# Kernel optimization log

Measured on AMD Instinct MI355X. Metric: run time of the kernel, lower is better.

Reference implementation:

```python
import jax, jax.numpy as jnp
import numpy as np

N = 50000      # nodes
E = 800000     # edges (before self-loops)
HEADS = 4
IN = 128
HID = 96
DH = HID // HEADS  # 24 per-head channels
G = 64         # graphs in batch
OUT = 3


def setup_inputs() -> dict:
    key = jax.random.key(0)
    ks = jax.random.split(key, 16)
    def w(k, shape, fan):
        return (jax.random.normal(k, shape, jnp.float32) * (fan ** -0.5)).astype(jnp.float32)
    x = jax.random.normal(ks[0], (N, IN), jnp.float32)
    edge_index = jax.random.randint(ks[1], (2, E), 0, N, dtype=jnp.int32)
    batch = jnp.sort(jax.random.randint(ks[2], (N,), 0, G, dtype=jnp.int32))
    return {
        'x': x, 'edge_index': edge_index, 'batch': batch, 'num_graphs': G,
        'W1': w(ks[3], (IN, HID), IN),
        'att_src1': w(ks[4], (HEADS, DH), DH),
        'att_dst1': w(ks[5], (HEADS, DH), DH),
        'b1': jnp.zeros((HID,), jnp.float32),
        'W2': w(ks[6], (HID, HID), HID),
        'att_src2': w(ks[7], (HEADS, DH), DH),
        'att_dst2': w(ks[8], (HEADS, DH), DH),
        'b2': jnp.zeros((HID,), jnp.float32),
        'g_w1': w(ks[9], (HID, HID // 2), HID),
        'g_b1': jnp.zeros((HID // 2,), jnp.float32),
        'g_w2': w(ks[10], (HID // 2, 1), HID // 2),
        'g_b2': jnp.zeros((1,), jnp.float32),
        'f_w1': w(ks[11], (HID, HID), HID),
        'f_b1': jnp.zeros((HID,), jnp.float32),
        'f_w2': w(ks[12], (HID, OUT), HID),
        'f_b2': jnp.zeros((OUT,), jnp.float32),
    }


def _gat_layer(x, src, dst, W, a_src, a_dst, b, n):
    # x: [n, F]; src/dst: [E'] (self-loops included). PyG GATConv math.
    h = (x @ W).reshape(n, HEADS, DH)                 # [n, H, d]
    alpha_s = jnp.sum(h * a_src[None], axis=-1)       # [n, H]
    alpha_d = jnp.sum(h * a_dst[None], axis=-1)       # [n, H]
    e = jax.nn.leaky_relu(alpha_s[src] + alpha_d[dst], 0.2)  # [E', H]
    # segment softmax over incoming edges of each dst node
    m = jax.ops.segment_max(e, dst, num_segments=n)   # [n, H]
    ex = jnp.exp(e - m[dst])
    denom = jax.ops.segment_sum(ex, dst, num_segments=n)
    alpha = ex / (denom[dst] + 1e-16)                 # [E', H]
    msg = h[src] * alpha[:, :, None]                  # [E', H, d]
    out = jax.ops.segment_sum(msg, dst, num_segments=n)
    return out.reshape(n, HEADS * DH) + b


def reference(x, edge_index, batch, num_graphs, W1, att_src1, att_dst1, b1,
              W2, att_src2, att_dst2, b2, g_w1, g_b1, g_w2, g_b2,
              f_w1, f_b1, f_w2, f_b2):
    n = x.shape[0]
    loops = jnp.arange(n, dtype=edge_index.dtype)
    src = jnp.concatenate([edge_index[0], loops])     # add self-loops (PyG default)
    dst = jnp.concatenate([edge_index[1], loops])
    h = jax.nn.elu(_gat_layer(x, src, dst, W1, att_src1, att_dst1, b1, n))
    h = jax.nn.elu(_gat_layer(h, src, dst, W2, att_src2, att_dst2, b2, n))
    # GlobalAttention pool: gate_nn -> softmax over batch segments -> weighted sum
    gate = (jax.nn.relu(h @ g_w1 + g_b1) @ g_w2 + g_b2)[:, 0]   # [n]
    gm = jax.ops.segment_max(gate, batch, num_segments=num_graphs)
    gm = jnp.where(jnp.isfinite(gm), gm, 0.0)
    ge = jnp.exp(gate - gm[batch])
    gden = jax.ops.segment_sum(ge, batch, num_segments=num_graphs)
    wgt = ge / (gden[batch] + 1e-16)                  # [n]
    pooled = jax.ops.segment_sum(h * wgt[:, None], batch, num_segments=num_graphs)  # [G, HID]
    return jax.nn.relu(pooled @ f_w1 + f_b1) @ f_w2 + f_b2   # [G, 3]
```

## Files before the change

kernel.cpp:

```cpp
#include <hip/hip_runtime.h>
#include <cmath>


__global__ void init_deg_kernel(int* __restrict__ deg, int n) {
    int i = blockIdx.x * blockDim.x + threadIdx.x;
    if (i < n) deg[i] = 1;
}

__global__ void hist_kernel(const int* __restrict__ dst, int* __restrict__ deg, int E) {
    int e = blockIdx.x * blockDim.x + threadIdx.x;
    if (e < E) atomicAdd(&deg[dst[e]], 1);
}

__global__ void scan_bsum_kernel(const int* __restrict__ deg, int* __restrict__ bsum, int n) {
    __shared__ int s[256];
    int t = threadIdx.x;
    int base = blockIdx.x * 1024;
    int sum = 0;
#pragma unroll
    for (int j = 0; j < 4; j++) {
        int i = base + j * 256 + t;
        if (i < n) sum += deg[i];
    }
    s[t] = sum;
    __syncthreads();
    for (int off = 128; off; off >>= 1) {
        if (t < off) s[t] += s[t + off];
        __syncthreads();
    }
    if (t == 0) bsum[blockIdx.x] = s[0];
}

__global__ void scan_bsum_scan_kernel(int* __restrict__ bsum, int nb,
                                      int* __restrict__ rowptr, int n) {
    __shared__ int s[256];
    int t = threadIdx.x;
    int v = (t < nb) ? bsum[t] : 0;
    s[t] = v;
    __syncthreads();
    for (int off = 1; off < 256; off <<= 1) {
        int x = (t >= off) ? s[t - off] : 0;
        __syncthreads();
        s[t] += x;
        __syncthreads();
    }
    if (t < nb) bsum[t] = s[t] - v;
    if (t == 255) rowptr[n] = s[255];
}

__global__ void scan_local_kernel(const int* __restrict__ deg, const int* __restrict__ bsum,
                                  int* __restrict__ rowptr, int* __restrict__ pos, int n) {
    __shared__ int s[256];
    int t = threadIdx.x;
    int base = blockIdx.x * 1024;
    int d[4];
    int sum = 0;
#pragma unroll
    for (int j = 0; j < 4; j++) {
        int i = base + t * 4 + j;
        d[j] = (i < n) ? deg[i] : 0;
        sum += d[j];
    }
    s[t] = sum;
    __syncthreads();
    for (int off = 1; off < 256; off <<= 1) {
        int x = (t >= off) ? s[t - off] : 0;
        __syncthreads();
        s[t] += x;
        __syncthreads();
    }
    int run = bsum[blockIdx.x] + s[t] - sum;
#pragma unroll
    for (int j = 0; j < 4; j++) {
        int i = base + t * 4 + j;
        if (i < n) { rowptr[i] = run; pos[i] = run; }
        run += d[j];
    }
}

__global__ void fill_kernel(const int* __restrict__ src, const int* __restrict__ dst,
                            int* __restrict__ pos, int* __restrict__ col, int E, int N) {
    int i = blockIdx.x * blockDim.x + threadIdx.x;
    if (i < E) {
        int p = atomicAdd(&pos[dst[i]], 1);
        col[p] = src[i];
    } else if (i < E + N) {
        int n = i - E;
        int p = atomicAdd(&pos[n], 1);
        col[p] = n;
    }
}

template<int K, int NCOL, int TN, int MODE>
__global__ __launch_bounds__(256)
void tiled_gemm_kernel(const float* __restrict__ X, const float* __restrict__ W,
                       const float* __restrict__ v1, const float* __restrict__ v2,
                       const float* __restrict__ v3,
                       float* __restrict__ H, float* __restrict__ AS, float* __restrict__ AD,
                       int n_nodes) {
    const int t = threadIdx.x;
    const int tx = t & 15, ty = t >> 4;
    const int c0 = tx * TN;
    const int m0 = ty * 4;
    const int node0 = blockIdx.x * 64;

    __shared__ float As[16][68];
    __shared__ float Bs[16][NCOL];

    float acc[4][TN];
#pragma unroll
    for (int i = 0; i < 4; i++)
#pragma unroll
        for (int j = 0; j < TN; j++) acc[i][j] = 0.f;

    const int am = t >> 2, akq = t & 3;

    for (int kb = 0; kb < K; kb += 16) {
        float4 av = make_float4(0.f, 0.f, 0.f, 0.f);
        int anode = node0 + am;
        if (anode < n_nodes)
            av = *reinterpret_cast<const float4*>(X + (size_t)anode * K + kb + akq * 4);
        As[akq * 4 + 0][am] = av.x;
        As[akq * 4 + 1][am] = av.y;
        As[akq * 4 + 2][am] = av.z;
        As[akq * 4 + 3][am] = av.w;
        {
            const float4* wsrc = reinterpret_cast<const float4*>(W + (size_t)kb * NCOL);
            float4* bdst = reinterpret_cast<float4*>(&Bs[0][0]);
            for (int i = t; i < 16 * NCOL / 4; i += 256) bdst[i] = wsrc[i];
        }
        __syncthreads();
#pragma unroll
        for (int k = 0; k < 16; k++) {
            float4 a4 = *reinterpret_cast<const float4*>(&As[k][m0]);
            float a[4] = {a4.x, a4.y, a4.z, a4.w};
            float b[TN];
            if constexpr ((TN & 1) == 0) {
#pragma unroll
                for (int j = 0; j < TN / 2; j++) {
                    float2 b2 = *reinterpret_cast<const float2*>(&Bs[k][c0 + 2 * j]);
                    b[2 * j] = b2.x; b[2 * j + 1] = b2.y;
                }
            } else {
#pragma unroll
                for (int j = 0; j < TN; j++) b[j] = Bs[k][c0 + j];
            }
#pragma unroll
            for (int i = 0; i < 4; i++)
#pragma unroll
                for (int j = 0; j < TN; j++)
                    acc[i][j] = fmaf(a[i], b[j], acc[i][j]);
        }
        __syncthreads();
    }

    if constexpr (MODE == 0) {
        __shared__ float s_as[64][16];
        __shared__ float s_ad[64][16];
#pragma unroll
        for (int i = 0; i < 4; i++) {
            int node = node0 + m0 + i;
            float asp = 0.f, adp = 0.f;
#pragma unroll
            for (int j = 0; j < TN; j++) {
                asp = fmaf(acc[i][j], v1[c0 + j], asp);
                adp = fmaf(acc[i][j], v2[c0 + j], adp);
            }
            s_as[m0 + i][tx] = asp;
            s_ad[m0 + i][tx] = adp;
            if (node < n_nodes) {
#pragma unroll
                for (int j = 0; j < TN / 2; j++) {
                    float2 o;
                    o.x = acc[i][2 * j]; o.y = acc[i][2 * j + 1];
                    *reinterpret_cast<float2*>(H + (size_t)node * NCOL + c0 + 2 * j) = o;
                }
            }
        }
        __syncthreads();
        int m = t >> 2, head = t & 3;
        int node = node0 + m;
        if (node < n_nodes) {
            float s1 = s_as[m][head * 4 + 0] + s_as[m][head * 4 + 1]
                     + s_as[m][head * 4 + 2] + s_as[m][head * 4 + 3];
            float s2 = s_ad[m][head * 4 + 0] + s_ad[m][head * 4 + 1]
                     + s_ad[m][head * 4 + 2] + s_ad[m][head * 4 + 3];
            AS[(size_t)node * 4 + head] = s1;
            AD[(size_t)node * 4 + head] = s2;
        }
    } else {
        __shared__ float s_g[64][16];
#pragma unroll
        for (int i = 0; i < 4; i++) {
            float p = 0.f;
#pragma unroll
            for (int j = 0; j < TN; j++) {
                float a = acc[i][j] + v1[c0 + j];
                a = fmaxf(a, 0.f);
                p = fmaf(a, v2[c0 + j], p);
            }
            s_g[m0 + i][tx] = p;
        }
        __syncthreads();
        if (t < 64) {
            int node = node0 + t;
            if (node < n_nodes) {
                float s = 0.f;
#pragma unroll
                for (int j = 0; j < 16; j++) s += s_g[t][j];
                H[node] = s + v3[0];
            }
        }
    }
}

__global__ __launch_bounds__(256)
void gat_agg_wave_kernel(const float* __restrict__ H, const float* __restrict__ AS,
                         const float* __restrict__ AD, const int* __restrict__ rowptr,
                         const int* __restrict__ col, const float* __restrict__ bias,
                         float* __restrict__ OUT, int n_nodes) {
    int wid = threadIdx.x >> 6;
    int lane = threadIdx.x & 63;
    int n = blockIdx.x * 4 + wid;
    if (n >= n_nodes) return;
    int beg = rowptr[n];
    int deg = rowptr[n + 1] - beg;

    int h = lane & 3;
    int slot = lane >> 2;
    float ad_n = AD[(size_t)n * 4 + h];

    float mymax = -INFINITY;
    for (int i = slot; i < deg; i += 16) {
        int s = col[beg + i];
        float v = AS[(size_t)s * 4 + h] + ad_n;
        v = v > 0.f ? v : 0.2f * v;
        mymax = fmaxf(mymax, v);
    }
#pragma unroll
    for (int m = 4; m <= 32; m <<= 1)
        mymax = fmaxf(mymax, __shfl_xor(mymax, m, 64));
    float m_h = mymax;

    int c = lane;
    bool cown = c < 48;
    int head_c = cown ? (c / 12) : 0;
    const float2* __restrict__ Hc = reinterpret_cast<const float2*>(H) + c;

    float denom_part = 0.f;
    float2 acc0 = make_float2(0.f, 0.f), acc1 = make_float2(0.f, 0.f);
    float2 acc2 = make_float2(0.f, 0.f), acc3 = make_float2(0.f, 0.f);

    for (int base = 0; base < deg; base += 16) {
        int ce = base + slot;
        int s_e = 0;
        float ex = 0.f;
        if (ce < deg) {
            s_e = col[beg + ce];
            float v = AS[(size_t)s_e * 4 + h] + ad_n;
            v = v > 0.f ? v : 0.2f * v;
            ex = __expf(v - m_h);
        }
        denom_part += ex;
        int cnt = min(16, deg - base);

        int sbv[16];
        float wv[16];
#pragma unroll
        for (int i = 0; i < 16; i++) {
            sbv[i] = __shfl(s_e, i * 4, 64);
            wv[i]  = __shfl(ex,  i * 4 + head_c, 64);
        }

#pragma unroll
        for (int g = 0; g < 16; g += 4) {
            if (g < cnt && cown) {
                float2 v0 = Hc[(size_t)sbv[g + 0] * 48];
                float2 v1 = Hc[(size_t)sbv[g + 1] * 48];
                float2 v2 = Hc[(size_t)sbv[g + 2] * 48];
                float2 v3 = Hc[(size_t)sbv[g + 3] * 48];
                acc0.x = fmaf(v0.x, wv[g + 0], acc0.x);
                acc0.y = fmaf(v0.y, wv[g + 0], acc0.y);
                acc1.x = fmaf(v1.x, wv[g + 1], acc1.x);
                acc1.y = fmaf(v1.y, wv[g + 1], acc1.y);
                acc2.x = fmaf(v2.x, wv[g + 2], acc2.x);
                acc2.y = fmaf(v2.y, wv[g + 2], acc2.y);
                acc3.x = fmaf(v3.x, wv[g + 3], acc3.x);
                acc3.y = fmaf(v3.y, wv[g + 3], acc3.y);
            }
        }
    }

#pragma unroll
    for (int m = 4; m <= 32; m <<= 1)
        denom_part += __shfl_xor(denom_part, m, 64);
    float den = __shfl(denom_part, head_c, 64);

    if (cown) {
        float2 acc;
        acc.x = (acc0.x + acc1.x) + (acc2.x + acc3.x);
        acc.y = (acc0.y + acc1.y) + (acc2.y + acc3.y);
        float2 b2 = reinterpret_cast<const float2*>(bias)[c];
        float inv = 1.f / (den + 1e-16f);
        float ox = acc.x * inv + b2.x;
        float oy = acc.y * inv + b2.y;
        ox = ox > 0.f ? ox : (__expf(ox) - 1.f);
        oy = oy > 0.f ? oy : (__expf(oy) - 1.f);
        reinterpret_cast<float2*>(OUT)[(size_t)n * 48 + c] = make_float2(ox, oy);
    }
}

__device__ __forceinline__ int lower_bound_dev(const int* __restrict__ arr, int n, int key) {
    int lo = 0, hi = n;
    while (lo < hi) {
        int mid = (lo + hi) >> 1;
        if (arr[mid] < key) lo = mid + 1; else hi = mid;
    }
    return lo;
}

__global__ void gate_stats_kernel(const float* __restrict__ gate, const int* __restrict__ batch,
                                  int n_nodes, float* __restrict__ gm_out,
                                  float* __restrict__ inv_gden_out, float* __restrict__ pooled) {
    int g = blockIdx.x, t = threadIdx.x;
    if (t < 96) pooled[(size_t)g * 96 + t] = 0.f;
    __shared__ int sb, se;
    __shared__ float sred[256];
    if (t == 0) {
        sb = lower_bound_dev(batch, n_nodes, g);
        se = lower_bound_dev(batch, n_nodes, g + 1);
    }
    __syncthreads();
    int beg = sb, end = se;

    float mx = -INFINITY;
    for (int i = beg + t; i < end; i += 256) mx = fmaxf(mx, gate[i]);
    sred[t] = mx;
    __syncthreads();
    for (int off = 128; off; off >>= 1) {
        if (t < off) sred[t] = fmaxf(sred[t], sred[t + off]);
        __syncthreads();
    }
    float gm = sred[0];
    if (!isfinite(gm)) gm = 0.f;
    __syncthreads();

    float sm = 0.f;
    for (int i = beg + t; i < end; i += 256) sm += __expf(gate[i] - gm);
    sred[t] = sm;
    __syncthreads();
    for (int off = 128; off; off >>= 1) {
        if (t < off) sred[t] += sred[t + off];
        __syncthreads();
    }
    if (t == 0) {
        gm_out[g] = gm;
        inv_gden_out[g] = 1.f / (sred[0] + 1e-16f);
    }
}

__global__ __launch_bounds__(384)
void pool_accum_kernel(const float* __restrict__ H2, const float* __restrict__ gate,
                       const int* __restrict__ batch, const float* __restrict__ gm,
                       const float* __restrict__ inv_gden, int n_nodes,
                       float* __restrict__ pooled) {
    const int NPB = 256;
    int t = threadIdx.x;
    int group = t / 96;
    int c = t - group * 96;
    if (group >= 4) return;
    int nbeg = blockIdx.x * NPB;
    int nend = min(nbeg + NPB, n_nodes);

    float acc = 0.f;
    int curg = -1;
    for (int i = nbeg + group; i < nend; i += 4) {
        int g = batch[i];
        if (g != curg) {
            if (curg >= 0) atomicAdd(&pooled[(size_t)curg * 96 + c], acc);
            acc = 0.f;
            curg = g;
        }
        float w = __expf(gate[i] - gm[curg]) * inv_gden[curg];
        acc = fmaf(w, H2[(size_t)i * 96 + c], acc);
    }
    if (curg >= 0) atomicAdd(&pooled[(size_t)curg * 96 + c], acc);
}

__global__ void final_kernel(const float* __restrict__ pooled, const float* __restrict__ f_w1,
                             const float* __restrict__ f_b1, const float* __restrict__ f_w2,
                             const float* __restrict__ f_b2, float* __restrict__ out) {
    int g = blockIdx.x, t = threadIdx.x;
    __shared__ float sp[96], sh[96];
    sp[t] = pooled[(size_t)g * 96 + t];
    __syncthreads();
    float a = f_b1[t];
    for (int k = 0; k < 96; k++) a = fmaf(sp[k], f_w1[k * 96 + t], a);
    sh[t] = fmaxf(a, 0.f);
    __syncthreads();
    if (t < 3) {
        float o = f_b2[t];
        for (int k = 0; k < 96; k++) o = fmaf(sh[k], f_w2[k * 3 + t], o);
        out[g * 3 + t] = o;
    }
}

extern "C" void kernel_launch(void* const* d_in, const int* in_sizes, int n_in,
                              void* d_out, int out_size, void* d_ws, size_t ws_size,
                              hipStream_t stream) {
    const float* x    = (const float*)d_in[0];
    const int*   ei   = (const int*)d_in[1];
    const int*   batch= (const int*)d_in[2];
    const float* W1   = (const float*)d_in[4];
    const float* as1  = (const float*)d_in[5];
    const float* ad1  = (const float*)d_in[6];
    const float* b1   = (const float*)d_in[7];
    const float* W2   = (const float*)d_in[8];
    const float* as2  = (const float*)d_in[9];
    const float* ad2  = (const float*)d_in[10];
    const float* b2   = (const float*)d_in[11];
    const float* g_w1 = (const float*)d_in[12];
    const float* g_b1 = (const float*)d_in[13];
    const float* g_w2 = (const float*)d_in[14];
    const float* g_b2 = (const float*)d_in[15];
    const float* f_w1 = (const float*)d_in[16];
    const float* f_b1 = (const float*)d_in[17];
    const float* f_w2 = (const float*)d_in[18];
    const float* f_b2 = (const float*)d_in[19];
    float* out = (float*)d_out;

    int N = in_sizes[0] / 128;
    int E = in_sizes[1] / 2;
    int G = out_size / 3;
    const int* srcv = ei;
    const int* dstv = ei + E;

    char* p = (char*)d_ws;
    auto alloc = [&](size_t bytes) {
        char* q = p;
        p += (bytes + 255) & ~(size_t)255;
        return q;
    };
    float* hA    = (float*)alloc((size_t)N * 96 * 4);
    float* hB    = (float*)alloc((size_t)N * 96 * 4);
    float* AS    = (float*)alloc((size_t)N * 4 * 4);
    float* AD    = (float*)alloc((size_t)N * 4 * 4);
    float* gatev = (float*)alloc((size_t)N * 4);
    float* pooled= (float*)alloc((size_t)G * 96 * 4);
    float* gmv   = (float*)alloc((size_t)G * 4);
    float* invgd = (float*)alloc((size_t)G * 4);
    int*   deg   = (int*)alloc((size_t)N * 4);
    int*   pos   = (int*)alloc((size_t)N * 4);
    int*   rowptr= (int*)alloc(((size_t)N + 1) * 4);
    int*   bsum  = (int*)alloc((size_t)256 * 4);
    int*   col   = (int*)alloc((size_t)(E + N) * 4);

    const int B = 256;
    int gemm_blocks = (N + 63) / 64;
    int nb_scan = (N + 1023) / 1024;

    init_deg_kernel<<<(N + B - 1) / B, B, 0, stream>>>(deg, N);
    hist_kernel<<<(E + B - 1) / B, B, 0, stream>>>(dstv, deg, E);
    scan_bsum_kernel<<<nb_scan, 256, 0, stream>>>(deg, bsum, N);
    scan_bsum_scan_kernel<<<1, 256, 0, stream>>>(bsum, nb_scan, rowptr, N);
    scan_local_kernel<<<nb_scan, 256, 0, stream>>>(deg, bsum, rowptr, pos, N);
    fill_kernel<<<(E + N + B - 1) / B, B, 0, stream>>>(srcv, dstv, pos, col, E, N);

    tiled_gemm_kernel<128, 96, 6, 0><<<gemm_blocks, 256, 0, stream>>>(
        x, W1, as1, ad1, nullptr, hA, AS, AD, N);
    gat_agg_wave_kernel<<<(N + 3) / 4, 256, 0, stream>>>(hA, AS, AD, rowptr, col, b1, hB, N);
    tiled_gemm_kernel<96, 96, 6, 0><<<gemm_blocks, 256, 0, stream>>>(
        hB, W2, as2, ad2, nullptr, hA, AS, AD, N);
    gat_agg_wave_kernel<<<(N + 3) / 4, 256, 0, stream>>>(hA, AS, AD, rowptr, col, b2, hB, N);

    tiled_gemm_kernel<96, 48, 3, 1><<<gemm_blocks, 256, 0, stream>>>(
        hB, g_w1, g_b1, g_w2, g_b2, gatev, nullptr, nullptr, N);
    gate_stats_kernel<<<G, 256, 0, stream>>>(gatev, batch, N, gmv, invgd, pooled);
    pool_accum_kernel<<<(N + 255) / 256, 384, 0, stream>>>(
        hB, gatev, batch, gmv, invgd, N, pooled);
    final_kernel<<<G, 96, 0, stream>>>(pooled, f_w1, f_b1, f_w2, f_b2, out);
}
```

Measured before the change: 352.4 us.

## Split GAT aggregation into edge-score, edge-softmax and gather kernels

Replaces the fused per-node wave kernel, which computed edge logits twice (once for the max pass and once for exp), with three passes. The new passes are a per-edge score kernel using a stored destination array, a per-node-head softmax that writes normalized exponentials and inverse denominators, and a simpler gather kernel. The degree init kernel is also replaced by a memset, with the self-loop +1 folded into the scan. The split adds extra global traffic for edge weights (Etot*16 bytes written and read) plus two extra launches per layer. The softmax kernel's serial per-thread loops with strided access may be slow.

```diff
diff --git a/kernel.cpp b/kernel.cpp
--- a/kernel.cpp
+++ b/kernel.cpp
@@ -1,11 +1,6 @@
 #include <hip/hip_runtime.h>
 #include <cmath>
 
-
-__global__ void init_deg_kernel(int* __restrict__ deg, int n) {
-    int i = blockIdx.x * blockDim.x + threadIdx.x;
-    if (i < n) deg[i] = 1;
-}
 
 __global__ void hist_kernel(const int* __restrict__ dst, int* __restrict__ deg, int E) {
     int e = blockIdx.x * blockDim.x + threadIdx.x;
@@ -20,7 +15,7 @@
 #pragma unroll
     for (int j = 0; j < 4; j++) {
         int i = base + j * 256 + t;
-        if (i < n) sum += deg[i];
+        if (i < n) sum += deg[i] + 1;
     }
     s[t] = sum;
     __syncthreads();
@@ -58,7 +53,7 @@
 #pragma unroll
     for (int j = 0; j < 4; j++) {
         int i = base + t * 4 + j;
-        d[j] = (i < n) ? deg[i] : 0;
+        d[j] = (i < n) ? deg[i] + 1 : 0;
         sum += d[j];
     }
     s[t] = sum;
@@ -79,15 +74,19 @@
 }
 
 __global__ void fill_kernel(const int* __restrict__ src, const int* __restrict__ dst,
-                            int* __restrict__ pos, int* __restrict__ col, int E, int N) {
+                            int* __restrict__ pos, int* __restrict__ col,
+                            int* __restrict__ edst, int E, int N) {
     int i = blockIdx.x * blockDim.x + threadIdx.x;
     if (i < E) {
-        int p = atomicAdd(&pos[dst[i]], 1);
+        int d = dst[i];
+        int p = atomicAdd(&pos[d], 1);
         col[p] = src[i];
+        edst[p] = d;
     } else if (i < E + N) {
         int n = i - E;
         int p = atomicAdd(&pos[n], 1);
         col[p] = n;
+        edst[p] = n;
     }
 }
 
@@ -214,96 +213,90 @@
     }
 }
 
+__global__ void edge_score_kernel(const float4* __restrict__ AS4, const float4* __restrict__ AD4,
+                                  const int* __restrict__ col, const int* __restrict__ edst,
+                                  float4* __restrict__ ew4, int Etot) {
+    int e = blockIdx.x * blockDim.x + threadIdx.x;
+    if (e >= Etot) return;
+    float4 a = AS4[col[e]];
+    float4 b = AD4[edst[e]];
+    float4 v;
+    v.x = a.x + b.x; v.y = a.y + b.y; v.z = a.z + b.z; v.w = a.w + b.w;
+    v.x = v.x > 0.f ? v.x : 0.2f * v.x;
+    v.y = v.y > 0.f ? v.y : 0.2f * v.y;
+    v.z = v.z > 0.f ? v.z : 0.2f * v.z;
+    v.w = v.w > 0.f ? v.w : 0.2f * v.w;
+    ew4[e] = v;
+}
+
+__global__ void edge_softmax_kernel(float* __restrict__ ew, const int* __restrict__ rowptr,
+                                    float* __restrict__ invden, int n_nodes) {
+    int tid = blockIdx.x * blockDim.x + threadIdx.x;
+    int node = tid >> 2, h = tid & 3;
+    if (node >= n_nodes) return;
+    int beg = rowptr[node], end = rowptr[node + 1];
+    float mx = -INFINITY;
+    for (int e = beg; e < end; ++e) mx = fmaxf(mx, ew[(size_t)e * 4 + h]);
+    float sum = 0.f;
+    for (int e = beg; e < end; ++e) {
+        float x = __expf(ew[(size_t)e * 4 + h] - mx);
+        ew[(size_t)e * 4 + h] = x;
+        sum += x;
+    }
+    invden[(size_t)node * 4 + h] = 1.f / (sum + 1e-16f);
+}
+
 __global__ __launch_bounds__(256)
-void gat_agg_wave_kernel(const float* __restrict__ H, const float* __restrict__ AS,
-                         const float* __restrict__ AD, const int* __restrict__ rowptr,
-                         const int* __restrict__ col, const float* __restrict__ bias,
-                         float* __restrict__ OUT, int n_nodes) {
-    int wid = threadIdx.x >> 6;
-    int lane = threadIdx.x & 63;
+void gat_gather_kernel(const float* __restrict__ H, const float* __restrict__ ew,
+                       const float* __restrict__ invden, const int* __restrict__ rowptr,
+                       const int* __restrict__ col, const float* __restrict__ bias,
+                       float* __restrict__ OUT, int n_nodes) {
+    int wid = threadIdx.x >> 6, lane = threadIdx.x & 63;
     int n = blockIdx.x * 4 + wid;
     if (n >= n_nodes) return;
-    int beg = rowptr[n];
-    int deg = rowptr[n + 1] - beg;
-
-    int h = lane & 3;
-    int slot = lane >> 2;
-    float ad_n = AD[(size_t)n * 4 + h];
-
-    float mymax = -INFINITY;
-    for (int i = slot; i < deg; i += 16) {
-        int s = col[beg + i];
-        float v = AS[(size_t)s * 4 + h] + ad_n;
-        v = v > 0.f ? v : 0.2f * v;
-        mymax = fmaxf(mymax, v);
-    }
-#pragma unroll
-    for (int m = 4; m <= 32; m <<= 1)
-        mymax = fmaxf(mymax, __shfl_xor(mymax, m, 64));
-    float m_h = mymax;
-
+    int beg = rowptr[n], end = rowptr[n + 1];
     int c = lane;
     bool cown = c < 48;
     int head_c = cown ? (c / 12) : 0;
     const float2* __restrict__ Hc = reinterpret_cast<const float2*>(H) + c;
 
-    float denom_part = 0.f;
-    float2 acc0 = make_float2(0.f, 0.f), acc1 = make_float2(0.f, 0.f);
-    float2 acc2 = make_float2(0.f, 0.f), acc3 = make_float2(0.f, 0.f);
-
-    for (int base = 0; base < deg; base += 16) {
-        int ce = base + slot;
-        int s_e = 0;
-        float ex = 0.f;
-        if (ce < deg) {
-            s_e = col[beg + ce];
-            float v = AS[(size_t)s_e * 4 + h] + ad_n;
-            v = v > 0.f ? v : 0.2f * v;
-            ex = __expf(v - m_h);
-        }
-        denom_part += ex;
-        int cnt = min(16, deg - base);
-
-        int sbv[16];
-        float wv[16];
-#pragma unroll
-        for (int i = 0; i < 16; i++) {
-            sbv[i] = __shfl(s_e, i * 4, 64);
-            wv[i]  = __shfl(ex,  i * 4 + head_c, 64);
-        }
-
-#pragma unroll
-        for (int g = 0; g < 16; g += 4) {
-            if (g < cnt && cown) {
-                float2 v0 = Hc[(size_t)sbv[g + 0] * 48];
-                float2 v1 = Hc[(size_t)sbv[g + 1] * 48];
-                float2 v2 = Hc[(size_t)sbv[g + 2] * 48];
-                float2 v3 = Hc[(size_t)sbv[g + 3] * 48];
-                acc0.x = fmaf(v0.x, wv[g + 0], acc0.x);
-                acc0.y = fmaf(v0.y, wv[g + 0], acc0.y);
-                acc1.x = fmaf(v1.x, wv[g + 1], acc1.x);
-                acc1.y = fmaf(v1.y, wv[g + 1], acc1.y);
-                acc2.x = fmaf(v2.x, wv[g + 2], acc2.x);
-                acc2.y = fmaf(v2.y, wv[g + 2], acc2.y);
-                acc3.x = fmaf(v3.x, wv[g + 3], acc3.x);
-                acc3.y = fmaf(v3.y, wv[g + 3], acc3.y);
-            }
-        }
-    }
-
-#pragma unroll
-    for (int m = 4; m <= 32; m <<= 1)
-        denom_part += __shfl_xor(denom_part, m, 64);
-    float den = __shfl(denom_part, head_c, 64);
+    float2 acc[8];
+#pragma unroll
+    for (int j = 0; j < 8; j++) acc[j] = make_float2(0.f, 0.f);
+
+    for (int base = beg; base < end; base += 8) {
+        int m = end - base;
+        int s[8];
+        float w[8];
+#pragma unroll
+        for (int j = 0; j < 8; j++) {
+            if (j < m) {
+                s[j] = col[base + j];
+                w[j] = ew[(size_t)(base + j) * 4 + head_c];
+            }
+        }
+        if (cown) {
+#pragma unroll
+            for (int j = 0; j < 8; j++) {
+                if (j < m) {
+                    float2 v = Hc[(size_t)s[j] * 48];
+                    acc[j].x = fmaf(v.x, w[j], acc[j].x);
+                    acc[j].y = fmaf(v.y, w[j], acc[j].y);
+                }
+            }
+        }
+    }
 
     if (cown) {
-        float2 acc;
-        acc.x = (acc0.x + acc1.x) + (acc2.x + acc3.x);
-        acc.y = (acc0.y + acc1.y) + (acc2.y + acc3.y);
+        float2 a;
+        a.x = ((acc[0].x + acc[1].x) + (acc[2].x + acc[3].x))
+            + ((acc[4].x + acc[5].x) + (acc[6].x + acc[7].x));
+        a.y = ((acc[0].y + acc[1].y) + (acc[2].y + acc[3].y))
+            + ((acc[4].y + acc[5].y) + (acc[6].y + acc[7].y));
+        float inv = invden[(size_t)n * 4 + head_c];
         float2 b2 = reinterpret_cast<const float2*>(bias)[c];
-        float inv = 1.f / (den + 1e-16f);
-        float ox = acc.x * inv + b2.x;
-        float oy = acc.y * inv + b2.y;
+        float ox = a.x * inv + b2.x;
+        float oy = a.y * inv + b2.y;
         ox = ox > 0.f ? ox : (__expf(ox) - 1.f);
         oy = oy > 0.f ? oy : (__expf(oy) - 1.f);
         reinterpret_cast<float2*>(OUT)[(size_t)n * 48 + c] = make_float2(ox, oy);
@@ -432,6 +425,7 @@
     int N = in_sizes[0] / 128;
     int E = in_sizes[1] / 2;
     int G = out_size / 3;
+    int Etot = E + N;
     const int* srcv = ei;
     const int* dstv = ei + E;
 
@@ -445,6 +439,7 @@
     float* hB    = (float*)alloc((size_t)N * 96 * 4);
     float* AS    = (float*)alloc((size_t)N * 4 * 4);
     float* AD    = (float*)alloc((size_t)N * 4 * 4);
+    float* invden= (float*)alloc((size_t)N * 4 * 4);
     float* gatev = (float*)alloc((size_t)N * 4);
     float* pooled= (float*)alloc((size_t)G * 96 * 4);
     float* gmv   = (float*)alloc((size_t)G * 4);
@@ -453,25 +448,33 @@
     int*   pos   = (int*)alloc((size_t)N * 4);
     int*   rowptr= (int*)alloc(((size_t)N + 1) * 4);
     int*   bsum  = (int*)alloc((size_t)256 * 4);
-    int*   col   = (int*)alloc((size_t)(E + N) * 4);
+    int*   col   = (int*)alloc((size_t)Etot * 4);
+    int*   edst  = (int*)alloc((size_t)Etot * 4);
+    float* ew    = (float*)alloc((size_t)Etot * 4 * 4);
 
     const int B = 256;
     int gemm_blocks = (N + 63) / 64;
     int nb_scan = (N + 1023) / 1024;
 
-    init_deg_kernel<<<(N + B - 1) / B, B, 0, stream>>>(deg, N);
+    hipMemsetAsync(deg, 0, (size_t)N * 4, stream);
     hist_kernel<<<(E + B - 1) / B, B, 0, stream>>>(dstv, deg, E);
     scan_bsum_kernel<<<nb_scan, 256, 0, stream>>>(deg, bsum, N);
     scan_bsum_scan_kernel<<<1, 256, 0, stream>>>(bsum, nb_scan, rowptr, N);
     scan_local_kernel<<<nb_scan, 256, 0, stream>>>(deg, bsum, rowptr, pos, N);
-    fill_kernel<<<(E + N + B - 1) / B, B, 0, stream>>>(srcv, dstv, pos, col, E, N);
+    fill_kernel<<<(Etot + B - 1) / B, B, 0, stream>>>(srcv, dstv, pos, col, edst, E, N);
 
     tiled_gemm_kernel<128, 96, 6, 0><<<gemm_blocks, 256, 0, stream>>>(
         x, W1, as1, ad1, nullptr, hA, AS, AD, N);
-    gat_agg_wave_kernel<<<(N + 3) / 4, 256, 0, stream>>>(hA, AS, AD, rowptr, col, b1, hB, N);
+    edge_score_kernel<<<(Etot + B - 1) / B, B, 0, stream>>>(
+        (const float4*)AS, (const float4*)AD, col, edst, (float4*)ew, Etot);
+    edge_softmax_kernel<<<(4 * N + B - 1) / B, B, 0, stream>>>(ew, rowptr, invden, N);
+    gat_gather_kernel<<<(N + 3) / 4, 256, 0, stream>>>(hA, ew, invden, rowptr, col, b1, hB, N);
     tiled_gemm_kernel<96, 96, 6, 0><<<gemm_blocks, 256, 0, stream>>>(
         hB, W2, as2, ad2, nullptr, hA, AS, AD, N);
-    gat_agg_wave_kernel<<<(N + 3) / 4, 256, 0, stream>>>(hA, AS, AD, rowptr, col, b2, hB, N);
+    edge_score_kernel<<<(Etot + B - 1) / B, B, 0, stream>>>(
+        (const float4*)AS, (const float4*)AD, col, edst, (float4*)ew, Etot);
+    edge_softmax_kernel<<<(4 * N + B - 1) / B, B, 0, stream>>>(ew, rowptr, invden, N);
+    gat_gather_kernel<<<(N + 3) / 4, 256, 0, stream>>>(hA, ew, invden, rowptr, col, b2, hB, N);
 
     tiled_gemm_kernel<96, 48, 3, 1><<<gemm_blocks, 256, 0, stream>>>(
         hB, g_w1, g_b1, g_w2, g_b2, gatev, nullptr, nullptr, N);
```

New measurement: 394.7 us. +12.0%, slower.
